# Optimization experiments

Measured on AMD Instinct MI355X. Metric: run time of the kernel, lower is better.

Reference implementation:

```python
import jax, jax.numpy as jnp
import numpy as np

B, T, E, DH = 4, 4096, 1024, 128

def setup_inputs() -> dict:
    key = jax.random.key(0)
    k1, k2, k3, k4 = jax.random.split(key, 4)
    scale = 1.0 / np.sqrt(E)
    return {
        "norm_inputs": jax.random.normal(k1, (B, T, E), dtype=jnp.float32),
        "Wq": jax.random.normal(k2, (E, DH), dtype=jnp.float32) * scale,
        "Wk": jax.random.normal(k3, (E, DH), dtype=jnp.float32) * scale,
        "Wv": jax.random.normal(k4, (E, DH), dtype=jnp.float32) * scale,
    }

def reference(norm_inputs, Wq, Wk, Wv):
    # q,k,v: [B,T,DH]
    q = jnp.einsum("bte,ed->btd", norm_inputs, Wq)
    k = jnp.einsum("bte,ed->btd", norm_inputs, Wk)
    v = jnp.einsum("bte,ed->btd", norm_inputs, Wv)
    Tn = norm_inputs.shape[1]
    # scaled scores [B,T,T]
    scores = jnp.einsum("bqd,bkd->bqk", q, k) / jnp.sqrt(jnp.asarray(q.shape[-1], q.dtype))
    causal = jnp.tril(jnp.ones((Tn, Tn), dtype=bool))
    scores = jnp.where(causal, scores, -jnp.inf)
    attn = jax.nn.softmax(scores, axis=-1)  # dropout p=0 -> identity
    return jnp.einsum("bqk,bkd->bqd", attn, v)
```

## Files before the change

### kernel.cpp

```cpp
#include <hip/hip_runtime.h>
#include <hip/hip_bf16.h>

#define NB 4
#define NT 4096
#define NE 1024
#define ND 128
#define QSCALE 0.12751741f

typedef unsigned u32x4 __attribute__((ext_vector_type(4)));
typedef float f32x4 __attribute__((ext_vector_type(4)));
typedef float f32x16 __attribute__((ext_vector_type(16)));
typedef __bf16 bf16x8 __attribute__((ext_vector_type(8)));
typedef unsigned short u16;

__device__ __forceinline__ unsigned cvt_pk_bf16(float lo, float hi) {
  unsigned r;
  asm("v_cvt_pk_bf16_f32 %0, %1, %2" : "=v"(r) : "v"(lo), "v"(hi));
  return r;
}
__device__ __forceinline__ void permswap(unsigned& a, unsigned& b) {
  asm("v_permlane32_swap_b32 %0, %1" : "+v"(a), "+v"(b));
}
__device__ __forceinline__ u16 f2bf(float f) {
  unsigned x = __float_as_uint(f);
  x += 0x7fffu + ((x >> 16) & 1u);
  return (u16)(x >> 16);
}
__device__ __forceinline__ f32x16 mfma32(bf16x8 a, bf16x8 b, f32x16 c) {
  return __builtin_amdgcn_mfma_f32_32x32x16_bf16(a, b, c, 0, 0, 0);
}
__device__ __forceinline__ bf16x8 ldb(const u16* p) {
  return *reinterpret_cast<const bf16x8*>(p);
}

__global__ void ah_prep(const float* __restrict__ Wq, const float* __restrict__ Wk,
                        const float* __restrict__ Wv, u16* __restrict__ wt) {
  const int g = blockIdx.x * 256 + threadIdx.x;
  const int m = g >> 14;
  const int r = g & 16383;
  const int d = r >> 7;
  const int ec = r & 127;
  const float* W = (m == 0) ? Wq : (m == 1) ? Wk : Wv;
  const float s = (m == 0) ? QSCALE : 1.0f;
  unsigned o[4];
#pragma unroll
  for (int i = 0; i < 4; ++i) {
    u16 a = f2bf(W[(size_t)(ec * 8 + 2 * i) * ND + d] * s);
    u16 b = f2bf(W[(size_t)(ec * 8 + 2 * i + 1) * ND + d] * s);
    o[i] = (unsigned)a | ((unsigned)b << 16);
  }
  u32x4 v; v[0] = o[0]; v[1] = o[1]; v[2] = o[2]; v[3] = o[3];
  *reinterpret_cast<u32x4*>(wt + (size_t)m * NE * ND + (size_t)d * NE + ec * 8) = v;
}

__global__ __launch_bounds__(256, 2) void ah_proj(
    const float* __restrict__ X, const u16* __restrict__ wt,
    u16* __restrict__ qb, u16* __restrict__ kb, u16* __restrict__ vtb) {
  const int bid = blockIdx.x;
  const int mat = bid % 3;
  const int mtile = bid / 3;
  const int row0 = mtile * 128;
  const int tid = threadIdx.x;
  const int w = tid >> 6;
  const int lane = tid & 63;
  const int l31 = lane & 31;
  const int h = lane >> 5;

  const u16* wmat = wt + (size_t)mat * NE * ND;
  const int rw = row0 + w * 32;
  const float* xrow = X + (size_t)(rw + l31) * NE + h * 8;

  f32x16 acc[4] = {};

#pragma unroll 2
  for (int e0 = 0; e0 < NE; e0 += 16) {
    f32x4 x0 = *reinterpret_cast<const f32x4*>(xrow + e0);
    f32x4 x1 = *reinterpret_cast<const f32x4*>(xrow + e0 + 4);
    u32x4 xw;
    xw[0] = cvt_pk_bf16(x0[0], x0[1]);
    xw[1] = cvt_pk_bf16(x0[2], x0[3]);
    xw[2] = cvt_pk_bf16(x1[0], x1[1]);
    xw[3] = cvt_pk_bf16(x1[2], x1[3]);
    bf16x8 xf = __builtin_bit_cast(bf16x8, xw);
    const u16* wrow = wmat + e0 + h * 8;
    if (mat < 2) {
#pragma unroll
      for (int d0 = 0; d0 < 4; ++d0) {
        bf16x8 wf = ldb(wrow + (size_t)(d0 * 32 + l31) * NE);
        acc[d0] = mfma32(xf, wf, acc[d0]);
      }
    } else {
#pragma unroll
      for (int d0 = 0; d0 < 4; ++d0) {
        bf16x8 wf = ldb(wrow + (size_t)(d0 * 32 + l31) * NE);
        acc[d0] = mfma32(wf, xf, acc[d0]);
      }
    }
  }

  if (mat < 2) {
    u16* dst = (mat == 0) ? qb : kb;
#pragma unroll
    for (int d0 = 0; d0 < 4; ++d0)
#pragma unroll
      for (int r = 0; r < 16; ++r) {
        const int trow = rw + (r & 3) + 8 * (r >> 2) + 4 * h;
        dst[(size_t)trow * ND + d0 * 32 + l31] = f2bf(acc[d0][r]);
      }
  } else {
    const int bb = rw >> 12;
    const int tt = (rw & 4095) + l31;
#pragma unroll
    for (int d0 = 0; d0 < 4; ++d0)
#pragma unroll
      for (int r = 0; r < 16; ++r) {
        const int d = d0 * 32 + (r & 3) + 8 * (r >> 2) + 4 * h;
        vtb[(size_t)bb * ND * NT + (size_t)d * NT + tt] = f2bf(acc[d0][r]);
      }
  }
}

__global__ __launch_bounds__(256, 2) void ah_attn(
    const u16* __restrict__ qg, const u16* __restrict__ kg,
    const u16* __restrict__ vtg, float* __restrict__ out) {
  __shared__ float smem_m[4][32];
  __shared__ float smem_l[4][32];
  __shared__ float smem_linv[32];
  __shared__ float smemO[128][33];

  const int bid = blockIdx.x;
  const int b = bid >> 6;
  const int p = bid & 63;
  const int tid = threadIdx.x;
  const int w = tid >> 6;
  const int lane = tid & 63;
  const int l31 = lane & 31;
  const int h = lane >> 5;

  const u16* Qb = qg + (size_t)b * NT * ND;
  const u16* Kb = kg + (size_t)b * NT * ND;
  const u16* VTb = vtg + (size_t)b * ND * NT;
  float* Ob = out + (size_t)b * NT * ND;

  for (int hf = 0; hf < 2; ++hf) {
    const int qt = hf ? (127 - p) : p;
    const int q0 = qt * 32;

    bf16x8 qf[8];
    {
      const u16* qrow = Qb + (size_t)(q0 + l31) * ND + h * 8;
#pragma unroll
      for (int s = 0; s < 8; ++s) qf[s] = ldb(qrow + s * 16);
    }

    float m_run = -1e30f, l_run = 0.f;
    f32x16 ot[4] = {};

    const int ntiles = qt + 1;
    for (int j = w; j < ntiles; j += 4) {
      const int k0 = j * 32;
      f32x16 sa = {};
      const u16* krow = Kb + (size_t)(k0 + l31) * ND + h * 8;
#pragma unroll
      for (int s = 0; s < 8; ++s) sa = mfma32(ldb(krow + s * 16), qf[s], sa);
      if (j == qt) {
#pragma unroll
        for (int r = 0; r < 16; ++r) {
          const int kk = (r & 3) + 8 * (r >> 2) + 4 * h;
          if (kk > l31) sa[r] = -1e30f;
        }
      }
      float mt = sa[0];
#pragma unroll
      for (int r = 1; r < 16; ++r) mt = fmaxf(mt, sa[r]);
      mt = fmaxf(mt, __shfl_xor(mt, 32));
      if (__any(mt > m_run + 8.f)) {
        const float mn = fmaxf(m_run, mt);
        const float f = __builtin_amdgcn_exp2f(m_run - mn);
        l_run *= f;
#pragma unroll
        for (int d0 = 0; d0 < 4; ++d0) ot[d0] *= f;
        m_run = mn;
      }
      float pr[16];
      float ps = 0.f;
#pragma unroll
      for (int r = 0; r < 16; ++r) {
        pr[r] = __builtin_amdgcn_exp2f(sa[r] - m_run);
        ps += pr[r];
      }
      ps += __shfl_xor(ps, 32);
      l_run += ps;
      unsigned pk[8];
#pragma unroll
      for (int i = 0; i < 8; ++i) pk[i] = cvt_pk_bf16(pr[2 * i], pr[2 * i + 1]);
      permswap(pk[0], pk[2]);
      permswap(pk[1], pk[3]);
      permswap(pk[4], pk[6]);
      permswap(pk[5], pk[7]);
      u32x4 t0, t1;
      t0[0] = pk[0]; t0[1] = pk[1]; t0[2] = pk[2]; t0[3] = pk[3];
      t1[0] = pk[4]; t1[1] = pk[5]; t1[2] = pk[6]; t1[3] = pk[7];
      bf16x8 pf0 = __builtin_bit_cast(bf16x8, t0);
      bf16x8 pf1 = __builtin_bit_cast(bf16x8, t1);
#pragma unroll
      for (int d0 = 0; d0 < 4; ++d0) {
        const u16* vrow = VTb + (size_t)(d0 * 32 + l31) * NT + k0 + h * 8;
        ot[d0] = mfma32(ldb(vrow), pf0, ot[d0]);
        ot[d0] = mfma32(ldb(vrow + 16), pf1, ot[d0]);
      }
    }

    if (h == 0) { smem_m[w][l31] = m_run; smem_l[w][l31] = l_run; }
    __syncthreads();
    float mstar = smem_m[0][l31];
#pragma unroll
    for (int wv = 1; wv < 4; ++wv) mstar = fmaxf(mstar, smem_m[wv][l31]);
    float lstar = 0.f;
#pragma unroll
    for (int wv = 0; wv < 4; ++wv)
      lstar += smem_l[wv][l31] * __builtin_amdgcn_exp2f(smem_m[wv][l31] - mstar);
    if (tid < 32) smem_linv[tid] = 1.0f / lstar;
    const float fw = __builtin_amdgcn_exp2f(m_run - mstar);
    for (int rnd = 0; rnd < 4; ++rnd) {
      if (w == rnd) {
#pragma unroll
        for (int d0 = 0; d0 < 4; ++d0)
#pragma unroll
          for (int r = 0; r < 16; ++r) {
            const int d = d0 * 32 + (r & 3) + 8 * (r >> 2) + 4 * h;
            const float v = ot[d0][r] * fw;
            if (rnd == 0) smemO[d][l31] = v;
            else smemO[d][l31] += v;
          }
      }
      __syncthreads();
    }
    {
      const int q = tid >> 3;
      const int dbase = (tid & 7) * 16;
      const float linv = smem_linv[q];
      float* orow = Ob + (size_t)(q0 + q) * ND + dbase;
#pragma unroll
      for (int c = 0; c < 4; ++c) {
        f32x4 v4;
#pragma unroll
        for (int e = 0; e < 4; ++e) v4[e] = smemO[dbase + c * 4 + e][q] * linv;
        *reinterpret_cast<f32x4*>(orow + c * 4) = v4;
      }
    }
    __syncthreads();
  }
}

extern "C" void kernel_launch(void* const* d_in, const int* in_sizes, int n_in,
                              void* d_out, int out_size, void* d_ws, size_t ws_size,
                              hipStream_t stream) {
  const float* X = (const float*)d_in[0];
  const float* Wq = (const float*)d_in[1];
  const float* Wk = (const float*)d_in[2];
  const float* Wv = (const float*)d_in[3];
  u16* ws = (u16*)d_ws;
  u16* wt = ws;
  u16* qb = wt + 393216;
  u16* kb = qb + 2097152;
  u16* vtb = kb + 2097152;
  float* out = (float*)d_out;

  ah_prep<<<192, 256, 0, stream>>>(Wq, Wk, Wv, wt);
  ah_proj<<<384, 256, 0, stream>>>(X, wt, qb, kb, vtb);
  ah_attn<<<256, 256, 0, stream>>>(qb, kb, vtb, out);
}
```

Before: 304.3 us.

## Restructure prep, projection and attention kernels for reuse and XCD-aware scheduling

The weight-prep kernel now transposes through shared memory, so its global loads and stores are coalesced. The projection kernel gives each block 32 rows and computes Q, K and V together, so each X tile is read once instead of three times. The attention kernel drops the paired-tile loop and launches one block per query tile, ordered longest-first and mapped by XCD so each batch stays on a pair of dies. Each wave also handles two key tiles per iteration to give more instruction-level parallelism. The trade-off is higher register pressure and the loss of the explicit causal load balancing inside each block.

```diff
diff --git a/kernel.cpp b/kernel.cpp
--- a/kernel.cpp
+++ b/kernel.cpp
@@ -32,45 +32,71 @@
 __device__ __forceinline__ bf16x8 ldb(const u16* p) {
   return *reinterpret_cast<const bf16x8*>(p);
 }
+__device__ __forceinline__ void pack_pf(const f32x16& pr, bf16x8& f0, bf16x8& f1) {
+  unsigned pk[8];
+#pragma unroll
+  for (int i = 0; i < 8; ++i) pk[i] = cvt_pk_bf16(pr[2 * i], pr[2 * i + 1]);
+  permswap(pk[0], pk[2]);
+  permswap(pk[1], pk[3]);
+  permswap(pk[4], pk[6]);
+  permswap(pk[5], pk[7]);
+  u32x4 t0, t1;
+  t0[0] = pk[0]; t0[1] = pk[1]; t0[2] = pk[2]; t0[3] = pk[3];
+  t1[0] = pk[4]; t1[1] = pk[5]; t1[2] = pk[6]; t1[3] = pk[7];
+  f0 = __builtin_bit_cast(bf16x8, t0);
+  f1 = __builtin_bit_cast(bf16x8, t1);
+}
 
 __global__ void ah_prep(const float* __restrict__ Wq, const float* __restrict__ Wk,
                         const float* __restrict__ Wv, u16* __restrict__ wt) {
-  const int g = blockIdx.x * 256 + threadIdx.x;
-  const int m = g >> 14;
-  const int r = g & 16383;
-  const int d = r >> 7;
-  const int ec = r & 127;
+  const int m = blockIdx.x >> 5;
+  const int r = blockIdx.x & 31;
+  const int e0 = (r >> 1) * 64;
+  const int d0 = (r & 1) * 64;
   const float* W = (m == 0) ? Wq : (m == 1) ? Wk : Wv;
   const float s = (m == 0) ? QSCALE : 1.0f;
-  unsigned o[4];
-#pragma unroll
-  for (int i = 0; i < 4; ++i) {
-    u16 a = f2bf(W[(size_t)(ec * 8 + 2 * i) * ND + d] * s);
-    u16 b = f2bf(W[(size_t)(ec * 8 + 2 * i + 1) * ND + d] * s);
-    o[i] = (unsigned)a | ((unsigned)b << 16);
-  }
-  u32x4 v; v[0] = o[0]; v[1] = o[1]; v[2] = o[2]; v[3] = o[3];
-  *reinterpret_cast<u32x4*>(wt + (size_t)m * NE * ND + (size_t)d * NE + ec * 8) = v;
+  __shared__ u16 lds[64][68];
+  const int t = threadIdx.x;
+  const int row = t >> 2;
+  const int c0 = (t & 3) * 16;
+  const float* src = W + (size_t)(e0 + row) * ND + d0 + c0;
+#pragma unroll
+  for (int i = 0; i < 16; i += 4) {
+    f32x4 v = *reinterpret_cast<const f32x4*>(src + i);
+#pragma unroll
+    for (int j = 0; j < 4; ++j) lds[c0 + i + j][row] = f2bf(v[j] * s);
+  }
+  __syncthreads();
+  const int d = t >> 2;
+  const int ec = (t & 3) * 16;
+  u16* dst = wt + (size_t)m * NE * ND + (size_t)(d0 + d) * NE + e0 + ec;
+  u32x4 o0, o1;
+#pragma unroll
+  for (int j = 0; j < 4; ++j)
+    o0[j] = (unsigned)lds[d][ec + 2 * j] | ((unsigned)lds[d][ec + 2 * j + 1] << 16);
+#pragma unroll
+  for (int j = 0; j < 4; ++j)
+    o1[j] = (unsigned)lds[d][ec + 8 + 2 * j] | ((unsigned)lds[d][ec + 8 + 2 * j + 1] << 16);
+  *reinterpret_cast<u32x4*>(dst) = o0;
+  *reinterpret_cast<u32x4*>(dst + 8) = o1;
 }
 
 __global__ __launch_bounds__(256, 2) void ah_proj(
     const float* __restrict__ X, const u16* __restrict__ wt,
     u16* __restrict__ qb, u16* __restrict__ kb, u16* __restrict__ vtb) {
-  const int bid = blockIdx.x;
-  const int mat = bid % 3;
-  const int mtile = bid / 3;
-  const int row0 = mtile * 128;
+  const int row0 = blockIdx.x * 32;
   const int tid = threadIdx.x;
   const int w = tid >> 6;
   const int lane = tid & 63;
   const int l31 = lane & 31;
   const int h = lane >> 5;
 
-  const u16* wmat = wt + (size_t)mat * NE * ND;
-  const int rw = row0 + w * 32;
-  const float* xrow = X + (size_t)(rw + l31) * NE + h * 8;
-
-  f32x16 acc[4] = {};
+  const float* xrow = X + (size_t)(row0 + l31) * NE + h * 8;
+  const u16* wpQ = wt + (size_t)(w * 32 + l31) * NE + h * 8;
+  const u16* wpK = wpQ + (size_t)NE * ND;
+  const u16* wpV = wpK + (size_t)NE * ND;
+
+  f32x16 accQ = {}, accK = {}, accV = {};
 
 #pragma unroll 2
   for (int e0 = 0; e0 < NE; e0 += 16) {
@@ -82,41 +108,24 @@
     xw[2] = cvt_pk_bf16(x1[0], x1[1]);
     xw[3] = cvt_pk_bf16(x1[2], x1[3]);
     bf16x8 xf = __builtin_bit_cast(bf16x8, xw);
-    const u16* wrow = wmat + e0 + h * 8;
-    if (mat < 2) {
-#pragma unroll
-      for (int d0 = 0; d0 < 4; ++d0) {
-        bf16x8 wf = ldb(wrow + (size_t)(d0 * 32 + l31) * NE);
-        acc[d0] = mfma32(xf, wf, acc[d0]);
-      }
-    } else {
-#pragma unroll
-      for (int d0 = 0; d0 < 4; ++d0) {
-        bf16x8 wf = ldb(wrow + (size_t)(d0 * 32 + l31) * NE);
-        acc[d0] = mfma32(wf, xf, acc[d0]);
-      }
-    }
-  }
-
-  if (mat < 2) {
-    u16* dst = (mat == 0) ? qb : kb;
-#pragma unroll
-    for (int d0 = 0; d0 < 4; ++d0)
-#pragma unroll
-      for (int r = 0; r < 16; ++r) {
-        const int trow = rw + (r & 3) + 8 * (r >> 2) + 4 * h;
-        dst[(size_t)trow * ND + d0 * 32 + l31] = f2bf(acc[d0][r]);
-      }
-  } else {
-    const int bb = rw >> 12;
-    const int tt = (rw & 4095) + l31;
-#pragma unroll
-    for (int d0 = 0; d0 < 4; ++d0)
-#pragma unroll
-      for (int r = 0; r < 16; ++r) {
-        const int d = d0 * 32 + (r & 3) + 8 * (r >> 2) + 4 * h;
-        vtb[(size_t)bb * ND * NT + (size_t)d * NT + tt] = f2bf(acc[d0][r]);
-      }
+    accQ = mfma32(xf, ldb(wpQ + e0), accQ);
+    accK = mfma32(xf, ldb(wpK + e0), accK);
+    accV = mfma32(ldb(wpV + e0), xf, accV);
+  }
+
+  const int col = w * 32 + l31;
+#pragma unroll
+  for (int r = 0; r < 16; ++r) {
+    const int trow = row0 + (r & 3) + 8 * (r >> 2) + 4 * h;
+    qb[(size_t)trow * ND + col] = f2bf(accQ[r]);
+    kb[(size_t)trow * ND + col] = f2bf(accK[r]);
+  }
+  const int bb = row0 >> 12;
+  const int tt = (row0 & 4095) + l31;
+#pragma unroll
+  for (int r = 0; r < 16; ++r) {
+    const int d = w * 32 + (r & 3) + 8 * (r >> 2) + 4 * h;
+    vtb[(size_t)bb * ND * NT + (size_t)d * NT + tt] = f2bf(accV[r]);
   }
 }
 
@@ -129,8 +138,11 @@
   __shared__ float smemO[128][33];
 
   const int bid = blockIdx.x;
-  const int b = bid >> 6;
-  const int p = bid & 63;
+  const int xcd = bid & 7;
+  const int slot = bid >> 3;
+  const int b = xcd >> 1;
+  const int qt = 127 - (slot * 2 + (xcd & 1));
+  const int q0 = qt * 32;
   const int tid = threadIdx.x;
   const int w = tid >> 6;
   const int lane = tid & 63;
@@ -142,114 +154,127 @@
   const u16* VTb = vtg + (size_t)b * ND * NT;
   float* Ob = out + (size_t)b * NT * ND;
 
-  for (int hf = 0; hf < 2; ++hf) {
-    const int qt = hf ? (127 - p) : p;
-    const int q0 = qt * 32;
-
-    bf16x8 qf[8];
-    {
-      const u16* qrow = Qb + (size_t)(q0 + l31) * ND + h * 8;
-#pragma unroll
-      for (int s = 0; s < 8; ++s) qf[s] = ldb(qrow + s * 16);
-    }
-
-    float m_run = -1e30f, l_run = 0.f;
-    f32x16 ot[4] = {};
-
-    const int ntiles = qt + 1;
-    for (int j = w; j < ntiles; j += 4) {
-      const int k0 = j * 32;
-      f32x16 sa = {};
-      const u16* krow = Kb + (size_t)(k0 + l31) * ND + h * 8;
-#pragma unroll
-      for (int s = 0; s < 8; ++s) sa = mfma32(ldb(krow + s * 16), qf[s], sa);
-      if (j == qt) {
+  bf16x8 qf[8];
+  {
+    const u16* qrow = Qb + (size_t)(q0 + l31) * ND + h * 8;
+#pragma unroll
+    for (int s = 0; s < 8; ++s) qf[s] = ldb(qrow + s * 16);
+  }
+
+  float m_run = -1e30f, l_run = 0.f;
+  f32x16 ot[4] = {};
+
+  const int ntiles = qt + 1;
+  for (int j0 = w; j0 < ntiles; j0 += 8) {
+    const int j1 = j0 + 4;
+    const bool has1 = (j1 < ntiles);
+    const int k0 = j0 * 32;
+    const int k1 = has1 ? j1 * 32 : k0;
+    f32x16 sa = {}, sb = {};
+    const u16* krow0 = Kb + (size_t)(k0 + l31) * ND + h * 8;
+    const u16* krow1 = Kb + (size_t)(k1 + l31) * ND + h * 8;
+#pragma unroll
+    for (int s = 0; s < 8; ++s) {
+      sa = mfma32(ldb(krow0 + s * 16), qf[s], sa);
+      sb = mfma32(ldb(krow1 + s * 16), qf[s], sb);
+    }
+    if (j0 == qt) {
+#pragma unroll
+      for (int r = 0; r < 16; ++r) {
+        const int kk = (r & 3) + 8 * (r >> 2) + 4 * h;
+        if (kk > l31) sa[r] = -1e30f;
+      }
+    }
+    if (has1) {
+      if (j1 == qt) {
 #pragma unroll
         for (int r = 0; r < 16; ++r) {
           const int kk = (r & 3) + 8 * (r >> 2) + 4 * h;
-          if (kk > l31) sa[r] = -1e30f;
+          if (kk > l31) sb[r] = -1e30f;
         }
       }
-      float mt = sa[0];
-#pragma unroll
-      for (int r = 1; r < 16; ++r) mt = fmaxf(mt, sa[r]);
-      mt = fmaxf(mt, __shfl_xor(mt, 32));
-      if (__any(mt > m_run + 8.f)) {
-        const float mn = fmaxf(m_run, mt);
-        const float f = __builtin_amdgcn_exp2f(m_run - mn);
-        l_run *= f;
-#pragma unroll
-        for (int d0 = 0; d0 < 4; ++d0) ot[d0] *= f;
-        m_run = mn;
-      }
-      float pr[16];
-      float ps = 0.f;
-#pragma unroll
-      for (int r = 0; r < 16; ++r) {
-        pr[r] = __builtin_amdgcn_exp2f(sa[r] - m_run);
-        ps += pr[r];
-      }
-      ps += __shfl_xor(ps, 32);
-      l_run += ps;
-      unsigned pk[8];
-#pragma unroll
-      for (int i = 0; i < 8; ++i) pk[i] = cvt_pk_bf16(pr[2 * i], pr[2 * i + 1]);
-      permswap(pk[0], pk[2]);
-      permswap(pk[1], pk[3]);
-      permswap(pk[4], pk[6]);
-      permswap(pk[5], pk[7]);
-      u32x4 t0, t1;
-      t0[0] = pk[0]; t0[1] = pk[1]; t0[2] = pk[2]; t0[3] = pk[3];
-      t1[0] = pk[4]; t1[1] = pk[5]; t1[2] = pk[6]; t1[3] = pk[7];
-      bf16x8 pf0 = __builtin_bit_cast(bf16x8, t0);
-      bf16x8 pf1 = __builtin_bit_cast(bf16x8, t1);
-#pragma unroll
-      for (int d0 = 0; d0 < 4; ++d0) {
-        const u16* vrow = VTb + (size_t)(d0 * 32 + l31) * NT + k0 + h * 8;
-        ot[d0] = mfma32(ldb(vrow), pf0, ot[d0]);
-        ot[d0] = mfma32(ldb(vrow + 16), pf1, ot[d0]);
-      }
-    }
-
-    if (h == 0) { smem_m[w][l31] = m_run; smem_l[w][l31] = l_run; }
+    } else {
+#pragma unroll
+      for (int r = 0; r < 16; ++r) sb[r] = -1e30f;
+    }
+    float mt = sa[0];
+#pragma unroll
+    for (int r = 1; r < 16; ++r) mt = fmaxf(mt, sa[r]);
+#pragma unroll
+    for (int r = 0; r < 16; ++r) mt = fmaxf(mt, sb[r]);
+    mt = fmaxf(mt, __shfl_xor(mt, 32));
+    if (__any(mt > m_run + 8.f)) {
+      const float mn = fmaxf(m_run, mt);
+      const float f = __builtin_amdgcn_exp2f(m_run - mn);
+      l_run *= f;
+#pragma unroll
+      for (int d0 = 0; d0 < 4; ++d0) ot[d0] *= f;
+      m_run = mn;
+    }
+    float ps = 0.f;
+#pragma unroll
+    for (int r = 0; r < 16; ++r) {
+      sa[r] = __builtin_amdgcn_exp2f(sa[r] - m_run);
+      ps += sa[r];
+    }
+#pragma unroll
+    for (int r = 0; r < 16; ++r) {
+      sb[r] = __builtin_amdgcn_exp2f(sb[r] - m_run);
+      ps += sb[r];
+    }
+    ps += __shfl_xor(ps, 32);
+    l_run += ps;
+    bf16x8 pf0a, pf0b, pf1a, pf1b;
+    pack_pf(sa, pf0a, pf0b);
+    pack_pf(sb, pf1a, pf1b);
+#pragma unroll
+    for (int d0 = 0; d0 < 4; ++d0) {
+      const u16* vrow0 = VTb + (size_t)(d0 * 32 + l31) * NT + k0 + h * 8;
+      const u16* vrow1 = VTb + (size_t)(d0 * 32 + l31) * NT + k1 + h * 8;
+      ot[d0] = mfma32(ldb(vrow0), pf0a, ot[d0]);
+      ot[d0] = mfma32(ldb(vrow0 + 16), pf0b, ot[d0]);
+      ot[d0] = mfma32(ldb(vrow1), pf1a, ot[d0]);
+      ot[d0] = mfma32(ldb(vrow1 + 16), pf1b, ot[d0]);
+    }
+  }
+
+  if (h == 0) { smem_m[w][l31] = m_run; smem_l[w][l31] = l_run; }
+  __syncthreads();
+  float mstar = smem_m[0][l31];
+#pragma unroll
+  for (int wv = 1; wv < 4; ++wv) mstar = fmaxf(mstar, smem_m[wv][l31]);
+  float lstar = 0.f;
+#pragma unroll
+  for (int wv = 0; wv < 4; ++wv)
+    lstar += smem_l[wv][l31] * __builtin_amdgcn_exp2f(smem_m[wv][l31] - mstar);
+  if (tid < 32) smem_linv[tid] = 1.0f / lstar;
+  const float fw = __builtin_amdgcn_exp2f(m_run - mstar);
+  for (int rnd = 0; rnd < 4; ++rnd) {
+    if (w == rnd) {
+#pragma unroll
+      for (int d0 = 0; d0 < 4; ++d0)
+#pragma unroll
+        for (int r = 0; r < 16; ++r) {
+          const int d = d0 * 32 + (r & 3) + 8 * (r >> 2) + 4 * h;
+          const float v = ot[d0][r] * fw;
+          if (rnd == 0) smemO[d][l31] = v;
+          else smemO[d][l31] += v;
+        }
+    }
     __syncthreads();
-    float mstar = smem_m[0][l31];
-#pragma unroll
-    for (int wv = 1; wv < 4; ++wv) mstar = fmaxf(mstar, smem_m[wv][l31]);
-    float lstar = 0.f;
-#pragma unroll
-    for (int wv = 0; wv < 4; ++wv)
-      lstar += smem_l[wv][l31] * __builtin_amdgcn_exp2f(smem_m[wv][l31] - mstar);
-    if (tid < 32) smem_linv[tid] = 1.0f / lstar;
-    const float fw = __builtin_amdgcn_exp2f(m_run - mstar);
-    for (int rnd = 0; rnd < 4; ++rnd) {
-      if (w == rnd) {
-#pragma unroll
-        for (int d0 = 0; d0 < 4; ++d0)
-#pragma unroll
-          for (int r = 0; r < 16; ++r) {
-            const int d = d0 * 32 + (r & 3) + 8 * (r >> 2) + 4 * h;
-            const float v = ot[d0][r] * fw;
-            if (rnd == 0) smemO[d][l31] = v;
-            else smemO[d][l31] += v;
-          }
-      }
-      __syncthreads();
-    }
-    {
-      const int q = tid >> 3;
-      const int dbase = (tid & 7) * 16;
-      const float linv = smem_linv[q];
-      float* orow = Ob + (size_t)(q0 + q) * ND + dbase;
-#pragma unroll
-      for (int c = 0; c < 4; ++c) {
-        f32x4 v4;
-#pragma unroll
-        for (int e = 0; e < 4; ++e) v4[e] = smemO[dbase + c * 4 + e][q] * linv;
-        *reinterpret_cast<f32x4*>(orow + c * 4) = v4;
-      }
-    }
-    __syncthreads();
+  }
+  {
+    const int q = tid >> 3;
+    const int dbase = (tid & 7) * 16;
+    const float linv = smem_linv[q];
+    float* orow = Ob + (size_t)(q0 + q) * ND + dbase;
+#pragma unroll
+    for (int c = 0; c < 4; ++c) {
+      f32x4 v4;
+#pragma unroll
+      for (int e = 0; e < 4; ++e) v4[e] = smemO[dbase + c * 4 + e][q] * linv;
+      *reinterpret_cast<f32x4*>(orow + c * 4) = v4;
+    }
   }
 }
 
@@ -267,7 +292,7 @@
   u16* vtb = kb + 2097152;
   float* out = (float*)d_out;
 
-  ah_prep<<<192, 256, 0, stream>>>(Wq, Wk, Wv, wt);
-  ah_proj<<<384, 256, 0, stream>>>(X, wt, qb, kb, vtb);
-  ah_attn<<<256, 256, 0, stream>>>(qb, kb, vtb, out);
-}
+  ah_prep<<<96, 256, 0, stream>>>(Wq, Wk, Wv, wt);
+  ah_proj<<<512, 256, 0, stream>>>(X, wt, qb, kb, vtb);
+  ah_attn<<<512, 256, 0, stream>>>(qb, kb, vtb, out);
+}
```

Result: faster. 265.2 us (-12.8%).
